# Kernel optimization log

Hardware: AMD Instinct MI355X
Metric: run time of the kernel (lower is better)

The kernel has to match this reference:

```python
import jax, jax.numpy as jnp
import numpy as np

N, IN_F, H, D = 3072, 512, 8, 64


def setup_inputs() -> dict:
    key = jax.random.key(0)
    k1, k2, k3, k4, k5 = jax.random.split(key, 5)
    x = jax.random.normal(k1, (N, IN_F), dtype=jnp.float32)
    adj = jax.random.randint(k2, (N, N), 0, 2, dtype=jnp.int32)
    # xavier-uniform-like scales
    s_W = (6.0 / (IN_F + H * D)) ** 0.5
    s_a = (6.0 / (H + D)) ** 0.5
    W = jax.random.uniform(k3, (H * D, IN_F), dtype=jnp.float32, minval=-s_W, maxval=s_W)
    a_src = jax.random.uniform(k4, (H, D), dtype=jnp.float32, minval=-s_a, maxval=s_a)
    a_dst = jax.random.uniform(k5, (H, D), dtype=jnp.float32, minval=-s_a, maxval=s_a)
    return {"x": x, "adj": adj, "W": W, "a_src": a_src, "a_dst": a_dst}


def reference(x, adj, W, a_src, a_dst):
    n = x.shape[0]
    Hh, d = a_src.shape
    h = (x @ W.T).reshape(n, Hh, d)                      # [n, H, d]
    e_src = jnp.einsum('nhd,hd->nh', h, a_src)           # [n, H]
    e_dst = jnp.einsum('nhd,hd->nh', h, a_dst)           # [n, H]
    e = e_src[:, None, :] + e_dst[None, :, :]            # [n, n, H], e[i,j]=src_i+dst_j
    e = jax.nn.leaky_relu(e, negative_slope=0.2)
    mask = (adj + jnp.eye(n, dtype=adj.dtype)) > 0       # [n, n]
    e = jnp.where(mask[:, :, None], e, -jnp.inf)
    alpha = jax.nn.softmax(e, axis=1)                    # softmax over j (neighbors)
    # out[i,h,d] = sum_j alpha[i,j,h] * h[j,h,d]  (dropout=0 / eval mode)
    out = jnp.einsum('ijh,jhd->ihd', alpha, h)
    return out.reshape(n, Hh * d)                        # concat=True
```

## Files before the change

### kernel.cpp

```cpp
#include <hip/hip_runtime.h>
#include <hip/hip_bf16.h>

typedef __bf16 bf16x8 __attribute__((ext_vector_type(8)));
typedef __bf16 bf16x4 __attribute__((ext_vector_type(4)));
typedef _Float16 half8 __attribute__((ext_vector_type(8)));
typedef _Float16 half2v __attribute__((ext_vector_type(2)));
typedef short s16x2 __attribute__((ext_vector_type(2)));
typedef float f32x4 __attribute__((ext_vector_type(4)));
typedef float f32x16 __attribute__((ext_vector_type(16)));

#define NROW 3072
#define NF 512
#define NH 8
#define ND 64
#define GEMM_BLOCKS 384
#define BP_BLOCKS 768
#define M0 8.0f

__device__ __forceinline__ void gat_ld4(float4 (&d)[4], const float* g, int c) {
#pragma unroll
    for (int t = 0; t < 4; ++t)
        d[t] = *reinterpret_cast<const float4*>(g + t * 8 * NF + c * 32);
}
__device__ __forceinline__ void gat_st4(__bf16* s, const float4 (&v)[4], int wslot) {
#pragma unroll
    for (int t = 0; t < 4; ++t) {
        bf16x4 w = { (__bf16)v[t].x, (__bf16)v[t].y, (__bf16)v[t].z, (__bf16)v[t].w };
        *reinterpret_cast<bf16x4*>(s + t * 320 + wslot) = w;
    }
}
__device__ __forceinline__ void gat_mfma2(const __bf16* sA, const __bf16* sB,
                                          int arow, int half, f32x16& acc) {
#pragma unroll
    for (int ks = 0; ks < 2; ++ks) {
        int q = ((ks << 1) | half) << 3;
        bf16x8 a = *reinterpret_cast<const bf16x8*>(sA + arow + q);
        bf16x8 b = *reinterpret_cast<const bf16x8*>(sB + arow + q);
        acc = __builtin_amdgcn_mfma_f32_32x32x16_bf16(a, b, acc, 0, 0, 0);
    }
}
__device__ __forceinline__ unsigned gat_pack16(unsigned v) {
    v = (v | (v >> 4)) & 0x00FF00FFu;
    v = (v | (v >> 8)) & 0x0000FFFFu;
    return v;
}

__global__ __launch_bounds__(256) void gat_gemm_bp(const float* __restrict__ x,
                                                   const float* __restrict__ W,
                                                   _Float16* __restrict__ hT,
                                                   const int* __restrict__ adj,
                                                   unsigned long long* __restrict__ bits64,
                                                   const float* __restrict__ a_src,
                                                   const float* __restrict__ a_dst,
                                                   float* __restrict__ e_srcT,
                                                   float* __restrict__ e_dstT) {
    __shared__ __align__(16) _Float16 smem[10240];
    __shared__ float ered[2][2][2][32];

    int tid = threadIdx.x;
    int wave = tid >> 6;
    int lane = tid & 63;

    if (blockIdx.x >= GEMM_BLOCKS) {
        int row = (blockIdx.x - GEMM_BLOCKS) * 4 + wave;
        const int4* p = reinterpret_cast<const int4*>(adj + (long)row * NROW) + lane;
        int4 v[12];
#pragma unroll
        for (int k = 0; k < 12; ++k) v[k] = p[k * 64];
        unsigned char* nib = reinterpret_cast<unsigned char*>(smem) + wave * 768;
#pragma unroll
        for (int k = 0; k < 12; ++k) {
            unsigned n = (v[k].x > 0 ? 1u : 0u) | (v[k].y > 0 ? 2u : 0u)
                       | (v[k].z > 0 ? 4u : 0u) | (v[k].w > 0 ? 8u : 0u);
            nib[k * 64 + lane] = (unsigned char)n;
        }
        int s = lane;
        if (s < 48) {
            uint4 q = *reinterpret_cast<const uint4*>(nib + s * 16);
            unsigned long long w = (unsigned long long)gat_pack16(q.x)
                                 | ((unsigned long long)gat_pack16(q.y) << 16)
                                 | ((unsigned long long)gat_pack16(q.z) << 32)
                                 | ((unsigned long long)gat_pack16(q.w) << 48);
            if (s == (row >> 6)) w |= 1ull << (row & 63);
            bits64[(long)row * 48 + s] = w;
        }
        return;
    }

    int b = blockIdx.x;
    int i0 = (b >> 3) * 64;
    int o0 = (b & 7) * 64;
    int head = b & 7;
    int half = lane >> 5;
    int l31 = lane & 31;
    int wr = wave >> 1;
    int wc = wave & 1;

    __bf16* sAw = reinterpret_cast<__bf16*>(smem) + wave * 1280;
    __bf16* sBw = reinterpret_cast<__bf16*>(smem) + 5120 + wave * 1280;

    int lr = lane >> 3;
    int lc = (lane & 7) * 4;
    const float* gA = x + (long)(i0 + wr * 32 + lr) * NF + lc;
    const float* gB = W + (long)(o0 + wc * 32 + lr) * NF + lc;
    int wslot = lr * 40 + lc;

    float4 Ae[4], Be[4], Ao[4], Bo[4];
    gat_ld4(Ae, gA, 0); gat_ld4(Be, gB, 0);
    gat_st4(sAw, Ae, wslot); gat_st4(sBw, Be, wslot);
    gat_ld4(Ao, gA, 1); gat_ld4(Bo, gB, 1);
    gat_ld4(Ae, gA, 2); gat_ld4(Be, gB, 2);

    f32x16 acc = {};
    int arow = l31 * 40;

#pragma unroll
    for (int cc = 0; cc < 8; ++cc) {
        int c0 = cc * 2, c1 = c0 + 1;
        gat_mfma2(sAw, sBw, arow, half, acc);
        gat_st4(sAw, Ao, wslot); gat_st4(sBw, Bo, wslot);
        if (c0 + 3 < 16) { gat_ld4(Ao, gA, c0 + 3); gat_ld4(Bo, gB, c0 + 3); }
        gat_mfma2(sAw, sBw, arow, half, acc);
        if (c1 + 1 < 16) {
            gat_st4(sAw, Ae, wslot); gat_st4(sBw, Be, wslot);
            if (c1 + 3 < 16) { gat_ld4(Ae, gA, c1 + 3); gat_ld4(Be, gB, c1 + 3); }
        }
    }

    _Float16* tt = smem + wave * 1280;
#pragma unroll
    for (int reg = 0; reg < 16; ++reg) {
        int rowl = (reg & 3) + 8 * (reg >> 2) + 4 * half;
        tt[rowl * 40 + l31] = (_Float16)acc[reg];
    }
    int orow = lane >> 1;
    int li = (lane & 1) * 16;
    half8 h0, h1;
#pragma unroll
    for (int t = 0; t < 8; ++t) h0[t] = tt[(li + t) * 40 + orow];
#pragma unroll
    for (int t = 0; t < 8; ++t) h1[t] = tt[(li + 8 + t) * 40 + orow];
    _Float16* op = hT + (long)(o0 + wc * 32 + orow) * NROW + i0 + wr * 32 + li;
    *reinterpret_cast<half8*>(op) = h0;
    *reinterpret_cast<half8*>(op + 8) = h1;

    half8 hv0 = *reinterpret_cast<const half8*>(tt + l31 * 40 + half * 16);
    half8 hv1 = *reinterpret_cast<const half8*>(tt + l31 * 40 + half * 16 + 8);
    const float* ap = a_src + head * ND + wc * 32 + half * 16;
    const float* dp = a_dst + head * ND + wc * 32 + half * 16;
    float4 as0 = *reinterpret_cast<const float4*>(ap);
    float4 as1 = *reinterpret_cast<const float4*>(ap + 4);
    float4 as2 = *reinterpret_cast<const float4*>(ap + 8);
    float4 as3 = *reinterpret_cast<const float4*>(ap + 12);
    float4 ad0 = *reinterpret_cast<const float4*>(dp);
    float4 ad1 = *reinterpret_cast<const float4*>(dp + 4);
    float4 ad2 = *reinterpret_cast<const float4*>(dp + 8);
    float4 ad3 = *reinterpret_cast<const float4*>(dp + 12);
    float ps = 0.f, pd = 0.f;
    ps += (float)hv0[0]*as0.x + (float)hv0[1]*as0.y + (float)hv0[2]*as0.z + (float)hv0[3]*as0.w;
    ps += (float)hv0[4]*as1.x + (float)hv0[5]*as1.y + (float)hv0[6]*as1.z + (float)hv0[7]*as1.w;
    ps += (float)hv1[0]*as2.x + (float)hv1[1]*as2.y + (float)hv1[2]*as2.z + (float)hv1[3]*as2.w;
    ps += (float)hv1[4]*as3.x + (float)hv1[5]*as3.y + (float)hv1[6]*as3.z + (float)hv1[7]*as3.w;
    pd += (float)hv0[0]*ad0.x + (float)hv0[1]*ad0.y + (float)hv0[2]*ad0.z + (float)hv0[3]*ad0.w;
    pd += (float)hv0[4]*ad1.x + (float)hv0[5]*ad1.y + (float)hv0[6]*ad1.z + (float)hv0[7]*ad1.w;
    pd += (float)hv1[0]*ad2.x + (float)hv1[1]*ad2.y + (float)hv1[2]*ad2.z + (float)hv1[3]*ad2.w;
    pd += (float)hv1[4]*ad3.x + (float)hv1[5]*ad3.y + (float)hv1[6]*ad3.z + (float)hv1[7]*ad3.w;
    ps += __shfl_xor(ps, 32, 64);
    pd += __shfl_xor(pd, 32, 64);
    if (half == 0) { ered[0][wr][wc][l31] = ps; ered[1][wr][wc][l31] = pd; }
    __syncthreads();
    if (wc == 0 && half == 0) {
        e_srcT[head * NROW + i0 + wr * 32 + l31] = ered[0][wr][0][l31] + ered[0][wr][1][l31];
        e_dstT[head * NROW + i0 + wr * 32 + l31] = ered[1][wr][0][l31] + ered[1][wr][1][l31];
    }
}

__global__ __launch_bounds__(256) void gat_attn(const unsigned* __restrict__ bits,
                                                const float* __restrict__ e_srcT,
                                                const float* __restrict__ e_dstT,
                                                const _Float16* __restrict__ hT,
                                                _Float16* __restrict__ num,
                                                float* __restrict__ den) {
    constexpr int JCHUNK = NROW / 4;
    constexpr int NC = JCHUNK / 64;
    __shared__ unsigned lds_P[JCHUNK / 2];
    __shared__ unsigned lds_Q[JCHUNK / 2];
    __shared__ __align__(16) _Float16 hbuf[2][4096];
    int b = blockIdx.x;
    int head = b & 7;
    int jc = (b >> 3) & 3;
    int i0 = (b >> 5) * 256;
    int jbase = jc * JCHUNK;
    int tid = threadIdx.x;
    int wave = tid >> 6;
    int lane = tid & 63;
    int half = lane >> 5;
    int l31 = lane & 31;

    for (int p = tid; p < JCHUNK / 2; p += 256) {
        float t0 = e_dstT[head * NROW + jbase + 2 * p] - M0;
        float t1 = e_dstT[head * NROW + jbase + 2 * p + 1] - M0;
        half2v P = { (_Float16)__expf(t0), (_Float16)__expf(t1) };
        half2v Q = { (_Float16)__expf(0.2f * t0), (_Float16)__expf(0.2f * t1) };
        lds_P[p] = __builtin_bit_cast(unsigned, P);
        lds_Q[p] = __builtin_bit_cast(unsigned, Q);
    }

    int irowA = i0 + wave * 32 + l31;
    int irowB = irowA + 128;
    float uA = e_srcT[head * NROW + irowA] + M0;
    float uB = e_srcT[head * NROW + irowB] + M0;
    float RfA = fminf(__expf(-0.8f * uA), 60000.f);
    float RfB = fminf(__expf(-0.8f * uB), 60000.f);
    _Float16 RhA = (_Float16)RfA, RhB = (_Float16)RfB;
    half2v R2A = { RhA, RhA };
    half2v R2B = { RhB, RhB };
    const half8 ones8 = { (_Float16)1.f, (_Float16)1.f, (_Float16)1.f, (_Float16)1.f,
                          (_Float16)1.f, (_Float16)1.f, (_Float16)1.f, (_Float16)1.f };
    const unsigned* browA = bits + (long)irowA * 96 + jc * (JCHUNK / 32);
    const unsigned* browB = bits + (long)irowB * 96 + jc * (JCHUNK / 32);

    int s0 = tid, s1 = tid + 256;
    const _Float16* gp0 = hT + (head * ND + ((s0 >> 6) & 1) * 32 + (s0 & 31)) * NROW
                             + jbase + (s0 >> 7) * 16 + ((s0 >> 5) & 1) * 8;
    const _Float16* gp1 = hT + (head * ND + ((s1 >> 6) & 1) * 32 + (s1 & 31)) * NROW
                             + jbase + (s1 >> 7) * 16 + ((s1 >> 5) & 1) * 8;
    *reinterpret_cast<half8*>(&hbuf[0][tid * 8])         = *reinterpret_cast<const half8*>(gp0);
    *reinterpret_cast<half8*>(&hbuf[0][(tid + 256) * 8]) = *reinterpret_cast<const half8*>(gp1);
    __syncthreads();

    f32x16 acc0a = {}, acc1a = {}, acc2a = {};
    f32x16 acc0b = {}, acc1b = {}, acc2b = {};
    uint2 wmA = *reinterpret_cast<const uint2*>(browA);
    uint2 wmB = *reinterpret_cast<const uint2*>(browB);

    for (int k = 0; k < NC; ++k) {
        half8 st0, st1;
        uint2 wmnA = wmA, wmnB = wmB;
        bool more = (k + 1 < NC);
        if (more) {
            st0 = *reinterpret_cast<const half8*>(gp0 + (k + 1) * 64);
            st1 = *reinterpret_cast<const half8*>(gp1 + (k + 1) * 64);
            wmnA = *reinterpret_cast<const uint2*>(browA + (k + 1) * 2);
            wmnB = *reinterpret_cast<const uint2*>(browB + (k + 1) * 2);
        }
        const _Float16* hb = &hbuf[k & 1][0];
#pragma unroll
        for (int js = 0; js < 4; ++js) {
            int sh = (js & 1) * 16 + half * 8;
            unsigned w8A = (((js < 2) ? wmA.x : wmA.y) >> sh) & 0xffu;
            unsigned w8B = (((js < 2) ? wmB.x : wmB.y) >> sh) & 0xffu;
            unsigned long long S64A = ((unsigned long long)(w8A & 0x55u) << 15)
                                    | ((unsigned long long)(w8A & 0xAAu) << 30);
            unsigned long long S64B = ((unsigned long long)(w8B & 0x55u) << 15)
                                    | ((unsigned long long)(w8B & 0xAAu) << 30);
            uint4 Pv = *reinterpret_cast<const uint4*>(&lds_P[k * 32 + js * 8 + half * 4]);
            uint4 Qv = *reinterpret_cast<const uint4*>(&lds_Q[k * 32 + js * 8 + half * 4]);
            unsigned pr[4] = { Pv.x, Pv.y, Pv.z, Pv.w };
            unsigned qr[4] = { Qv.x, Qv.y, Qv.z, Qv.w };
            unsigned amA[4], amB[4];
#pragma unroll
            for (int t = 0; t < 4; ++t) {
                half2v pv = __builtin_bit_cast(half2v, pr[t]);
                half2v qv = __builtin_bit_cast(half2v, qr[t]);
                half2v mxA = __builtin_elementwise_max(pv, qv * R2A);
                half2v mxB = __builtin_elementwise_max(pv, qv * R2B);
                s16x2 mkA = __builtin_bit_cast(s16x2, (unsigned)(S64A >> (2 * t))) >> 15;
                s16x2 mkB = __builtin_bit_cast(s16x2, (unsigned)(S64B >> (2 * t))) >> 15;
                amA[t] = __builtin_bit_cast(unsigned, mxA) & __builtin_bit_cast(unsigned, mkA);
                amB[t] = __builtin_bit_cast(unsigned, mxB) & __builtin_bit_cast(unsigned, mkB);
            }
            uint4 m4a = { amA[0], amA[1], amA[2], amA[3] };
            uint4 m4b = { amB[0], amB[1], amB[2], amB[3] };
            half8 afA = __builtin_bit_cast(half8, m4a);
            half8 afB = __builtin_bit_cast(half8, m4b);
            half8 v0 = *reinterpret_cast<const half8*>(hb + (js * 128 + lane) * 8);
            half8 v1 = *reinterpret_cast<const half8*>(hb + (js * 128 + 64 + lane) * 8);
            acc0a = __builtin_amdgcn_mfma_f32_32x32x16_f16(afA, v0, acc0a, 0, 0, 0);
            acc1a = __builtin_amdgcn_mfma_f32_32x32x16_f16(afA, v1, acc1a, 0, 0, 0);
            acc2a = __builtin_amdgcn_mfma_f32_32x32x16_f16(afA, ones8, acc2a, 0, 0, 0);
            acc0b = __builtin_amdgcn_mfma_f32_32x32x16_f16(afB, v0, acc0b, 0, 0, 0);
            acc1b = __builtin_amdgcn_mfma_f32_32x32x16_f16(afB, v1, acc1b, 0, 0, 0);
            acc2b = __builtin_amdgcn_mfma_f32_32x32x16_f16(afB, ones8, acc2b, 0, 0, 0);
        }
        if (more) {
            *reinterpret_cast<half8*>(&hbuf[(k + 1) & 1][tid * 8])         = st0;
            *reinterpret_cast<half8*>(&hbuf[(k + 1) & 1][(tid + 256) * 8]) = st1;
        }
        wmA = wmnA;
        wmB = wmnB;
        __syncthreads();
    }

#pragma unroll
    for (int reg = 0; reg < 16; ++reg) {
        int rowl = (reg & 3) + 8 * (reg >> 2) + 4 * half;
        long rbaseA = (long)(jc * NROW + i0 + wave * 32 + rowl);
        long rbaseB = rbaseA + 128;
        if (l31 == 0) {
            den[rbaseA * NH + head] = acc2a[reg];
            den[rbaseB * NH + head] = acc2b[reg];
        }
        long obA = rbaseA * NF + head * ND + l31;
        long obB = rbaseB * NF + head * ND + l31;
        num[obA]      = (_Float16)acc0a[reg];
        num[obA + 32] = (_Float16)acc1a[reg];
        num[obB]      = (_Float16)acc0b[reg];
        num[obB + 32] = (_Float16)acc1b[reg];
    }
}

__global__ __launch_bounds__(256) void gat_final(const _Float16* __restrict__ num,
                                                 const float* __restrict__ den,
                                                 float* __restrict__ out) {
    int idx = (blockIdx.x * 256 + threadIdx.x) * 8;
    int i = idx >> 9;
    int c = idx & 511;
    int head = c >> 6;
    half8 n0 = *reinterpret_cast<const half8*>(num + (long)i * NF + c);
    half8 n1 = *reinterpret_cast<const half8*>(num + (long)(NROW + i) * NF + c);
    half8 n2 = *reinterpret_cast<const half8*>(num + (long)(2 * NROW + i) * NF + c);
    half8 n3 = *reinterpret_cast<const half8*>(num + (long)(3 * NROW + i) * NF + c);
    float ds = den[i * NH + head] + den[(NROW + i) * NH + head]
             + den[(2 * NROW + i) * NH + head] + den[(3 * NROW + i) * NH + head];
    float inv = 1.0f / fmaxf(ds, 1e-30f);
    float r0 = ((float)n0[0] + (float)n1[0] + (float)n2[0] + (float)n3[0]) * inv;
    float r1 = ((float)n0[1] + (float)n1[1] + (float)n2[1] + (float)n3[1]) * inv;
    float r2 = ((float)n0[2] + (float)n1[2] + (float)n2[2] + (float)n3[2]) * inv;
    float r3 = ((float)n0[3] + (float)n1[3] + (float)n2[3] + (float)n3[3]) * inv;
    float r4 = ((float)n0[4] + (float)n1[4] + (float)n2[4] + (float)n3[4]) * inv;
    float r5 = ((float)n0[5] + (float)n1[5] + (float)n2[5] + (float)n3[5]) * inv;
    float r6 = ((float)n0[6] + (float)n1[6] + (float)n2[6] + (float)n3[6]) * inv;
    float r7 = ((float)n0[7] + (float)n1[7] + (float)n2[7] + (float)n3[7]) * inv;
    float4 o0 = { r0, r1, r2, r3 };
    float4 o1 = { r4, r5, r6, r7 };
    *reinterpret_cast<float4*>(out + idx)     = o0;
    *reinterpret_cast<float4*>(out + idx + 4) = o1;
}

extern "C" void kernel_launch(void* const* d_in, const int* in_sizes, int n_in,
                              void* d_out, int out_size, void* d_ws, size_t ws_size,
                              hipStream_t stream) {
    const float* x_raw  = (const float*)d_in[0];
    const int*   adj    = (const int*)d_in[1];
    const float* W_raw  = (const float*)d_in[2];
    const float* as_raw = (const float*)d_in[3];
    const float* ad_raw = (const float*)d_in[4];
    float* out = (float*)d_out;

    char* ws = (char*)d_ws;
    _Float16* hT     = (_Float16*)(ws);
    float*    e_srcT = (float*)(ws + 3145728);
    float*    e_dstT = (float*)(ws + 3244032);
    unsigned* bits   = (unsigned*)(ws + 3342400);
    _Float16* num    = (_Float16*)(ws + 8192064);
    float*    den    = (float*)(ws + 20774976);

    gat_gemm_bp<<<GEMM_BLOCKS + BP_BLOCKS, 256, 0, stream>>>(x_raw, W_raw, hT, adj,
                                                             (unsigned long long*)bits,
                                                             as_raw, ad_raw,
                                                             e_srcT, e_dstT);
    gat_attn<<<12 * 4 * 8, 256, 0, stream>>>(bits, e_srcT, e_dstT, hT, num, den);
    gat_final<<<NROW * NF / 2048, 256, 0, stream>>>(num, den, out);
}
```

Measured before the change: 126.0 us.

## Drop j-split in attention kernel and normalize in-kernel, removing final reduction

The attention kernel no longer splits the neighbor dimension into four chunks with partial num/den buffers. Each block now covers 64 rows of one head over all 3072 neighbors, and the four waves split the row and d halves. Each block divides by the denominator and writes fp32 output directly, so the separate final kernel and its fp16 partial-sum traffic go away. The cost is that each wave now builds masked-weight fragments for a single row tile and recomputes the full P/Q table per block. The j-loop also runs longer per block, and there are the same 384 blocks but with less MFMA work per wave per iteration.

```diff
diff --git a/kernel.cpp b/kernel.cpp
--- a/kernel.cpp
+++ b/kernel.cpp
@@ -179,163 +179,103 @@
                                                 const float* __restrict__ e_srcT,
                                                 const float* __restrict__ e_dstT,
                                                 const _Float16* __restrict__ hT,
-                                                _Float16* __restrict__ num,
-                                                float* __restrict__ den) {
-    constexpr int JCHUNK = NROW / 4;
-    constexpr int NC = JCHUNK / 64;
-    __shared__ unsigned lds_P[JCHUNK / 2];
-    __shared__ unsigned lds_Q[JCHUNK / 2];
+                                                float* __restrict__ out) {
+    constexpr int NC = NROW / 64;
+    __shared__ unsigned lds_P[NROW / 2];
+    __shared__ unsigned lds_Q[NROW / 2];
     __shared__ __align__(16) _Float16 hbuf[2][4096];
     int b = blockIdx.x;
     int head = b & 7;
-    int jc = (b >> 3) & 3;
-    int i0 = (b >> 5) * 256;
-    int jbase = jc * JCHUNK;
+    int i0 = (b >> 3) * 64;
     int tid = threadIdx.x;
     int wave = tid >> 6;
     int lane = tid & 63;
     int half = lane >> 5;
     int l31 = lane & 31;
-
-    for (int p = tid; p < JCHUNK / 2; p += 256) {
-        float t0 = e_dstT[head * NROW + jbase + 2 * p] - M0;
-        float t1 = e_dstT[head * NROW + jbase + 2 * p + 1] - M0;
+    int wr = wave >> 1;
+    int wd = wave & 1;
+
+    for (int p = tid; p < NROW / 2; p += 256) {
+        float t0 = e_dstT[head * NROW + 2 * p] - M0;
+        float t1 = e_dstT[head * NROW + 2 * p + 1] - M0;
         half2v P = { (_Float16)__expf(t0), (_Float16)__expf(t1) };
         half2v Q = { (_Float16)__expf(0.2f * t0), (_Float16)__expf(0.2f * t1) };
         lds_P[p] = __builtin_bit_cast(unsigned, P);
         lds_Q[p] = __builtin_bit_cast(unsigned, Q);
     }
 
-    int irowA = i0 + wave * 32 + l31;
-    int irowB = irowA + 128;
-    float uA = e_srcT[head * NROW + irowA] + M0;
-    float uB = e_srcT[head * NROW + irowB] + M0;
-    float RfA = fminf(__expf(-0.8f * uA), 60000.f);
-    float RfB = fminf(__expf(-0.8f * uB), 60000.f);
-    _Float16 RhA = (_Float16)RfA, RhB = (_Float16)RfB;
-    half2v R2A = { RhA, RhA };
-    half2v R2B = { RhB, RhB };
+    int irow = i0 + wr * 32 + l31;
+    float u = e_srcT[head * NROW + irow] + M0;
+    float Rf = fminf(__expf(-0.8f * u), 60000.f);
+    _Float16 Rh = (_Float16)Rf;
+    half2v R2 = { Rh, Rh };
     const half8 ones8 = { (_Float16)1.f, (_Float16)1.f, (_Float16)1.f, (_Float16)1.f,
                           (_Float16)1.f, (_Float16)1.f, (_Float16)1.f, (_Float16)1.f };
-    const unsigned* browA = bits + (long)irowA * 96 + jc * (JCHUNK / 32);
-    const unsigned* browB = bits + (long)irowB * 96 + jc * (JCHUNK / 32);
+    const unsigned* brow = bits + (long)irow * 96;
 
     int s0 = tid, s1 = tid + 256;
     const _Float16* gp0 = hT + (head * ND + ((s0 >> 6) & 1) * 32 + (s0 & 31)) * NROW
-                             + jbase + (s0 >> 7) * 16 + ((s0 >> 5) & 1) * 8;
+                             + (s0 >> 7) * 16 + ((s0 >> 5) & 1) * 8;
     const _Float16* gp1 = hT + (head * ND + ((s1 >> 6) & 1) * 32 + (s1 & 31)) * NROW
-                             + jbase + (s1 >> 7) * 16 + ((s1 >> 5) & 1) * 8;
+                             + (s1 >> 7) * 16 + ((s1 >> 5) & 1) * 8;
     *reinterpret_cast<half8*>(&hbuf[0][tid * 8])         = *reinterpret_cast<const half8*>(gp0);
     *reinterpret_cast<half8*>(&hbuf[0][(tid + 256) * 8]) = *reinterpret_cast<const half8*>(gp1);
     __syncthreads();
 
-    f32x16 acc0a = {}, acc1a = {}, acc2a = {};
-    f32x16 acc0b = {}, acc1b = {}, acc2b = {};
-    uint2 wmA = *reinterpret_cast<const uint2*>(browA);
-    uint2 wmB = *reinterpret_cast<const uint2*>(browB);
+    f32x16 acc0 = {};
+    f32x16 acc2 = {};
+    uint2 wm = *reinterpret_cast<const uint2*>(brow);
 
     for (int k = 0; k < NC; ++k) {
         half8 st0, st1;
-        uint2 wmnA = wmA, wmnB = wmB;
+        uint2 wmn = wm;
         bool more = (k + 1 < NC);
         if (more) {
             st0 = *reinterpret_cast<const half8*>(gp0 + (k + 1) * 64);
             st1 = *reinterpret_cast<const half8*>(gp1 + (k + 1) * 64);
-            wmnA = *reinterpret_cast<const uint2*>(browA + (k + 1) * 2);
-            wmnB = *reinterpret_cast<const uint2*>(browB + (k + 1) * 2);
+            wmn = *reinterpret_cast<const uint2*>(brow + (k + 1) * 2);
         }
         const _Float16* hb = &hbuf[k & 1][0];
 #pragma unroll
         for (int js = 0; js < 4; ++js) {
             int sh = (js & 1) * 16 + half * 8;
-            unsigned w8A = (((js < 2) ? wmA.x : wmA.y) >> sh) & 0xffu;
-            unsigned w8B = (((js < 2) ? wmB.x : wmB.y) >> sh) & 0xffu;
-            unsigned long long S64A = ((unsigned long long)(w8A & 0x55u) << 15)
-                                    | ((unsigned long long)(w8A & 0xAAu) << 30);
-            unsigned long long S64B = ((unsigned long long)(w8B & 0x55u) << 15)
-                                    | ((unsigned long long)(w8B & 0xAAu) << 30);
+            unsigned w8 = (((js < 2) ? wm.x : wm.y) >> sh) & 0xffu;
+            unsigned long long S64 = ((unsigned long long)(w8 & 0x55u) << 15)
+                                   | ((unsigned long long)(w8 & 0xAAu) << 30);
             uint4 Pv = *reinterpret_cast<const uint4*>(&lds_P[k * 32 + js * 8 + half * 4]);
             uint4 Qv = *reinterpret_cast<const uint4*>(&lds_Q[k * 32 + js * 8 + half * 4]);
             unsigned pr[4] = { Pv.x, Pv.y, Pv.z, Pv.w };
             unsigned qr[4] = { Qv.x, Qv.y, Qv.z, Qv.w };
-            unsigned amA[4], amB[4];
+            unsigned am[4];
 #pragma unroll
             for (int t = 0; t < 4; ++t) {
                 half2v pv = __builtin_bit_cast(half2v, pr[t]);
                 half2v qv = __builtin_bit_cast(half2v, qr[t]);
-                half2v mxA = __builtin_elementwise_max(pv, qv * R2A);
-                half2v mxB = __builtin_elementwise_max(pv, qv * R2B);
-                s16x2 mkA = __builtin_bit_cast(s16x2, (unsigned)(S64A >> (2 * t))) >> 15;
-                s16x2 mkB = __builtin_bit_cast(s16x2, (unsigned)(S64B >> (2 * t))) >> 15;
-                amA[t] = __builtin_bit_cast(unsigned, mxA) & __builtin_bit_cast(unsigned, mkA);
-                amB[t] = __builtin_bit_cast(unsigned, mxB) & __builtin_bit_cast(unsigned, mkB);
+                half2v mx = __builtin_elementwise_max(pv, qv * R2);
+                s16x2 mk = __builtin_bit_cast(s16x2, (unsigned)(S64 >> (2 * t))) >> 15;
+                am[t] = __builtin_bit_cast(unsigned, mx) & __builtin_bit_cast(unsigned, mk);
             }
-            uint4 m4a = { amA[0], amA[1], amA[2], amA[3] };
-            uint4 m4b = { amB[0], amB[1], amB[2], amB[3] };
-            half8 afA = __builtin_bit_cast(half8, m4a);
-            half8 afB = __builtin_bit_cast(half8, m4b);
-            half8 v0 = *reinterpret_cast<const half8*>(hb + (js * 128 + lane) * 8);
-            half8 v1 = *reinterpret_cast<const half8*>(hb + (js * 128 + 64 + lane) * 8);
-            acc0a = __builtin_amdgcn_mfma_f32_32x32x16_f16(afA, v0, acc0a, 0, 0, 0);
-            acc1a = __builtin_amdgcn_mfma_f32_32x32x16_f16(afA, v1, acc1a, 0, 0, 0);
-            acc2a = __builtin_amdgcn_mfma_f32_32x32x16_f16(afA, ones8, acc2a, 0, 0, 0);
-            acc0b = __builtin_amdgcn_mfma_f32_32x32x16_f16(afB, v0, acc0b, 0, 0, 0);
-            acc1b = __builtin_amdgcn_mfma_f32_32x32x16_f16(afB, v1, acc1b, 0, 0, 0);
-            acc2b = __builtin_amdgcn_mfma_f32_32x32x16_f16(afB, ones8, acc2b, 0, 0, 0);
+            uint4 m4 = { am[0], am[1], am[2], am[3] };
+            half8 af = __builtin_bit_cast(half8, m4);
+            half8 v = *reinterpret_cast<const half8*>(hb + (js * 128 + wd * 64 + lane) * 8);
+            acc0 = __builtin_amdgcn_mfma_f32_32x32x16_f16(af, v, acc0, 0, 0, 0);
+            acc2 = __builtin_amdgcn_mfma_f32_32x32x16_f16(af, ones8, acc2, 0, 0, 0);
         }
         if (more) {
             *reinterpret_cast<half8*>(&hbuf[(k + 1) & 1][tid * 8])         = st0;
             *reinterpret_cast<half8*>(&hbuf[(k + 1) & 1][(tid + 256) * 8]) = st1;
         }
-        wmA = wmnA;
-        wmB = wmnB;
+        wm = wmn;
         __syncthreads();
     }
 
 #pragma unroll
     for (int reg = 0; reg < 16; ++reg) {
         int rowl = (reg & 3) + 8 * (reg >> 2) + 4 * half;
-        long rbaseA = (long)(jc * NROW + i0 + wave * 32 + rowl);
-        long rbaseB = rbaseA + 128;
-        if (l31 == 0) {
-            den[rbaseA * NH + head] = acc2a[reg];
-            den[rbaseB * NH + head] = acc2b[reg];
-        }
-        long obA = rbaseA * NF + head * ND + l31;
-        long obB = rbaseB * NF + head * ND + l31;
-        num[obA]      = (_Float16)acc0a[reg];
-        num[obA + 32] = (_Float16)acc1a[reg];
-        num[obB]      = (_Float16)acc0b[reg];
-        num[obB + 32] = (_Float16)acc1b[reg];
-    }
-}
-
-__global__ __launch_bounds__(256) void gat_final(const _Float16* __restrict__ num,
-                                                 const float* __restrict__ den,
-                                                 float* __restrict__ out) {
-    int idx = (blockIdx.x * 256 + threadIdx.x) * 8;
-    int i = idx >> 9;
-    int c = idx & 511;
-    int head = c >> 6;
-    half8 n0 = *reinterpret_cast<const half8*>(num + (long)i * NF + c);
-    half8 n1 = *reinterpret_cast<const half8*>(num + (long)(NROW + i) * NF + c);
-    half8 n2 = *reinterpret_cast<const half8*>(num + (long)(2 * NROW + i) * NF + c);
-    half8 n3 = *reinterpret_cast<const half8*>(num + (long)(3 * NROW + i) * NF + c);
-    float ds = den[i * NH + head] + den[(NROW + i) * NH + head]
-             + den[(2 * NROW + i) * NH + head] + den[(3 * NROW + i) * NH + head];
-    float inv = 1.0f / fmaxf(ds, 1e-30f);
-    float r0 = ((float)n0[0] + (float)n1[0] + (float)n2[0] + (float)n3[0]) * inv;
-    float r1 = ((float)n0[1] + (float)n1[1] + (float)n2[1] + (float)n3[1]) * inv;
-    float r2 = ((float)n0[2] + (float)n1[2] + (float)n2[2] + (float)n3[2]) * inv;
-    float r3 = ((float)n0[3] + (float)n1[3] + (float)n2[3] + (float)n3[3]) * inv;
-    float r4 = ((float)n0[4] + (float)n1[4] + (float)n2[4] + (float)n3[4]) * inv;
-    float r5 = ((float)n0[5] + (float)n1[5] + (float)n2[5] + (float)n3[5]) * inv;
-    float r6 = ((float)n0[6] + (float)n1[6] + (float)n2[6] + (float)n3[6]) * inv;
-    float r7 = ((float)n0[7] + (float)n1[7] + (float)n2[7] + (float)n3[7]) * inv;
-    float4 o0 = { r0, r1, r2, r3 };
-    float4 o1 = { r4, r5, r6, r7 };
-    *reinterpret_cast<float4*>(out + idx)     = o0;
-    *reinterpret_cast<float4*>(out + idx + 4) = o1;
+        float inv = 1.0f / fmaxf(acc2[reg], 1e-30f);
+        out[(long)(i0 + wr * 32 + rowl) * NF + head * ND + wd * 32 + l31]
+            = acc0[reg] * inv;
+    }
 }
 
 extern "C" void kernel_launch(void* const* d_in, const int* in_sizes, int n_in,
@@ -353,13 +293,10 @@
     float*    e_srcT = (float*)(ws + 3145728);
     float*    e_dstT = (float*)(ws + 3244032);
     unsigned* bits   = (unsigned*)(ws + 3342400);
-    _Float16* num    = (_Float16*)(ws + 8192064);
-    float*    den    = (float*)(ws + 20774976);
 
     gat_gemm_bp<<<GEMM_BLOCKS + BP_BLOCKS, 256, 0, stream>>>(x_raw, W_raw, hT, adj,
                                                              (unsigned long long*)bits,
                                                              as_raw, ad_raw,
                                                              e_srcT, e_dstT);
-    gat_attn<<<12 * 4 * 8, 256, 0, stream>>>(bits, e_srcT, e_dstT, hT, num, den);
-    gat_final<<<NROW * NF / 2048, 256, 0, stream>>>(num, den, out);
-}
+    gat_attn<<<48 * 8, 256, 0, stream>>>(bits, e_srcT, e_dstT, hT, out);
+}
```

Result: slower. 145.7 us (+15.6%).
